# Kernel optimization log

Measured on AMD Instinct MI355X. Metric: run time of the kernel, lower is better.

## Reference

```python
import jax, jax.numpy as jnp
import numpy as np

N_NODES = 50000
N_EDGES = 800000
IN_F = 512
OUT_F = 96
ALPHA = 0.1
ITERATIONS = 10
AVG_DEG = 16


def setup_inputs() -> dict:
    key = jax.random.key(0)
    k1, k2, k3, k4, k5 = jax.random.split(key, 5)
    x = jax.random.normal(k1, (N_NODES, IN_F), dtype=jnp.float32)
    # xavier_uniform with gain=1.414 over [IN_F, OUT_F]
    limit = 1.414 * np.sqrt(6.0 / (IN_F + OUT_F))
    weight = jax.random.uniform(k2, (IN_F, OUT_F), dtype=jnp.float32,
                                minval=-limit, maxval=limit)
    edge_src = jax.random.randint(k3, (N_EDGES,), 0, N_NODES, dtype=jnp.int32)
    edge_dst = jax.random.randint(k4, (N_EDGES,), 0, N_NODES, dtype=jnp.int32)
    # values scaled like a row-normalized adjacency for stable propagation
    edge_val = jax.random.uniform(k5, (N_EDGES,), dtype=jnp.float32) / AVG_DEG
    return {"x": x, "weight": weight, "edge_src": edge_src,
            "edge_dst": edge_dst, "edge_val": edge_val}


def _spmm(edge_src, edge_dst, edge_val, h):
    # out[i] = sum_{edges e with dst=i} val[e] * h[src[e]]
    gathered = h[edge_src] * edge_val[:, None]          # [E, OUT_F]
    return jax.ops.segment_sum(gathered, edge_dst, num_segments=N_NODES)


def reference(x, weight, edge_src, edge_dst, edge_val):
    support = x @ weight                                 # [N, OUT_F]
    prev = support
    def body(_, s):
        s = _spmm(edge_src, edge_dst, edge_val, s) * (1.0 - ALPHA) + prev * ALPHA
        return jax.nn.relu(s)
    return jax.lax.fori_loop(0, ITERATIONS, body, support)
```

## Files before the change

kernel.cpp:

```cpp
#include <hip/hip_runtime.h>

typedef unsigned int   uint;
typedef unsigned short ushort;
typedef __attribute__((ext_vector_type(8))) short bf16x8;
typedef __attribute__((ext_vector_type(4))) float f32x4;

#define N_NODES 50000
#define N_EDGES 800000
#define IN_F    512
#define OUT_F   96
#define SCAN_BLOCKS 196
#define TPN 12
#define DEGBINS 256

__device__ __forceinline__ float bflo(uint u) { return __uint_as_float(u << 16); }
__device__ __forceinline__ float bfhi(uint u) { return __uint_as_float(u & 0xffff0000u); }
__device__ __forceinline__ uint f2bf(float x) {
    uint u = __float_as_uint(x);
    return (u + 0x7fffu + ((u >> 16) & 1u)) >> 16;
}
__device__ __forceinline__ uint pack2bf(float lo, float hi) {
    return f2bf(lo) | (f2bf(hi) << 16);
}

__global__ __launch_bounds__(256) void wt_kernel(const float* __restrict__ w,
                                                 ushort* __restrict__ wTp) {
    int t = blockIdx.x * 256 + threadIdx.x;
    if (t < IN_F * OUT_F) {
        int k = t / OUT_F, c = t - k * OUT_F;
        wTp[(size_t)(k >> 5) * (OUT_F * 32) + c * 32 + (k & 31)] =
            (ushort)f2bf(w[t]);
    }
}

__global__ __launch_bounds__(64) void gemm_kernel(const float* __restrict__ x,
                                                  const ushort* __restrict__ wTp,
                                                  ushort* __restrict__ supB) {
    const int lane = threadIdx.x;
    const int m    = lane & 15;
    const int quad = lane >> 4;

    const int row  = blockIdx.x * 16 + m;
    const int arow = (row < N_NODES) ? row : (N_NODES - 1);
    const float*  xp = x + (size_t)arow * IN_F + quad * 8;
    const ushort* wp = wTp + (size_t)m * 32 + quad * 8;

    f32x4 acc[6];
    #pragma unroll
    for (int ct = 0; ct < 6; ++ct) acc[ct] = (f32x4){0.f, 0.f, 0.f, 0.f};

    float4 xA0 = *(const float4*)(xp);
    float4 xB0 = *(const float4*)(xp + 4);
    float4 xA1 = *(const float4*)(xp + 32);
    float4 xB1 = *(const float4*)(xp + 36);
    bf16x8 b[6];
    #pragma unroll
    for (int ct = 0; ct < 6; ++ct)
        b[ct] = *(const bf16x8*)(wp + ct * (16 * 32));

    #pragma unroll
    for (int it = 0; it < 16; ++it) {
        float4 nxa, nxb;
        bf16x8 nb[6];
        if (it + 2 < 16) {
            nxa = *(const float4*)(xp + (it + 2) * 32);
            nxb = *(const float4*)(xp + (it + 2) * 32 + 4);
        }
        if (it + 1 < 16) {
            const ushort* wpn = wp + (size_t)(it + 1) * (OUT_F * 32);
            #pragma unroll
            for (int ct = 0; ct < 6; ++ct)
                nb[ct] = *(const bf16x8*)(wpn + ct * (16 * 32));
        }
        union { uint u[4]; bf16x8 v; } af;
        af.u[0] = pack2bf(xA0.x, xA0.y); af.u[1] = pack2bf(xA0.z, xA0.w);
        af.u[2] = pack2bf(xB0.x, xB0.y); af.u[3] = pack2bf(xB0.z, xB0.w);
        #pragma unroll
        for (int ct = 0; ct < 6; ++ct)
            acc[ct] = __builtin_amdgcn_mfma_f32_16x16x32_bf16(af.v, b[ct],
                                                              acc[ct], 0, 0, 0);
        xA0 = xA1; xB0 = xB1; xA1 = nxa; xB1 = nxb;
        #pragma unroll
        for (int ct = 0; ct < 6; ++ct) b[ct] = nb[ct];
    }

    const int orow0 = blockIdx.x * 16 + quad * 4;
    #pragma unroll
    for (int ct = 0; ct < 6; ++ct) {
        #pragma unroll
        for (int r = 0; r < 4; ++r) {
            int gr = orow0 + r;
            if (gr < N_NODES)
                supB[(size_t)gr * OUT_F + ct * 16 + m] = (ushort)f2bf(acc[ct][r]);
        }
    }
}

__global__ void zero_kernel(int* __restrict__ p, int n) {
    int t = blockIdx.x * blockDim.x + threadIdx.x;
    if (t < n) p[t] = 0;
}

__global__ void hist_kernel(const int* __restrict__ dst, int* __restrict__ counts) {
    int e = blockIdx.x * blockDim.x + threadIdx.x;
    if (e < N_EDGES) atomicAdd(&counts[dst[e]], 1);
}

__global__ __launch_bounds__(256) void block_reduce_kernel(const int* __restrict__ counts,
                                                           int* __restrict__ blockSums) {
    __shared__ int s[256];
    int idx = blockIdx.x * 256 + threadIdx.x;
    s[threadIdx.x] = (idx < N_NODES) ? counts[idx] : 0;
    __syncthreads();
    for (int off = 128; off > 0; off >>= 1) {
        if (threadIdx.x < off) s[threadIdx.x] += s[threadIdx.x + off];
        __syncthreads();
    }
    if (threadIdx.x == 0) blockSums[blockIdx.x] = s[0];
}

__global__ __launch_bounds__(256) void scan_sums_kernel(int* __restrict__ blockSums,
                                                        int* __restrict__ blockOffs,
                                                        int* __restrict__ rowstart) {
    __shared__ int s[256];
    int t = threadIdx.x;
    s[t] = (t < SCAN_BLOCKS) ? blockSums[t] : 0;
    __syncthreads();
    for (int off = 1; off < 256; off <<= 1) {
        int v = (t >= off) ? s[t - off] : 0;
        __syncthreads();
        s[t] += v;
        __syncthreads();
    }
    if (t < SCAN_BLOCKS) blockOffs[t] = (t == 0) ? 0 : s[t - 1];
    if (t == 0) rowstart[N_NODES] = s[SCAN_BLOCKS - 1];
}

__global__ __launch_bounds__(256) void block_scan_kernel(const int* __restrict__ counts,
                                                         const int* __restrict__ blockOffs,
                                                         int* __restrict__ rowstart,
                                                         int* __restrict__ cursor,
                                                         int* __restrict__ deghist) {
    __shared__ int s[256];
    __shared__ int lh[DEGBINS];
    int t   = threadIdx.x;
    int idx = blockIdx.x * 256 + t;
    int v   = (idx < N_NODES) ? counts[idx] : 0;
    s[t]  = v;
    lh[t] = 0;
    __syncthreads();
    for (int off = 1; off < 256; off <<= 1) {
        int u = (t >= off) ? s[t - off] : 0;
        __syncthreads();
        s[t] += u;
        __syncthreads();
    }
    if (idx < N_NODES) {
        int excl = blockOffs[blockIdx.x] + s[t] - v;
        rowstart[idx] = excl;
        cursor[idx]   = excl;
        int d = v < (DEGBINS - 1) ? v : (DEGBINS - 1);
        atomicAdd(&lh[d], 1);
    }
    __syncthreads();
    if (lh[t] > 0) atomicAdd(&deghist[t], lh[t]);
}

__global__ __launch_bounds__(256) void degscan_kernel(const int* __restrict__ deghist,
                                                      int* __restrict__ degcur) {
    __shared__ int s[256];
    int t = threadIdx.x;
    int v = deghist[t];
    s[t] = v;
    __syncthreads();
    for (int off = 1; off < 256; off <<= 1) {
        int u = (t >= off) ? s[t - off] : 0;
        __syncthreads();
        s[t] += u;
        __syncthreads();
    }
    degcur[t] = s[t] - v;
}

__global__ __launch_bounds__(256) void degscatter_kernel(const int* __restrict__ counts,
                                                         int* __restrict__ degcur,
                                                         int* __restrict__ perm) {
    __shared__ int lhist[DEGBINS];
    __shared__ int lbase[DEGBINS];
    int t = threadIdx.x;
    lhist[t] = 0;
    __syncthreads();
    int i = blockIdx.x * 256 + t;
    int d = 0, lr = 0;
    bool valid = (i < N_NODES);
    if (valid) {
        d  = counts[i];
        if (d > DEGBINS - 1) d = DEGBINS - 1;
        lr = atomicAdd(&lhist[d], 1);
    }
    __syncthreads();
    if (lhist[t] > 0) lbase[t] = atomicAdd(&degcur[t], lhist[t]);
    __syncthreads();
    if (valid) perm[lbase[d] + lr] = i;
}

__global__ void scatter_kernel(const int* __restrict__ src, const int* __restrict__ dst,
                               const float* __restrict__ val, int* __restrict__ cursor,
                               uint* __restrict__ edgeE) {
    int e = blockIdx.x * blockDim.x + threadIdx.x;
    if (e < N_EDGES) {
        int d   = dst[e];
        int pos = atomicAdd(&cursor[d], 1);
        edgeE[pos] = (f2bf(val[e]) << 16) | (uint)src[e];
    }
}

__device__ __forceinline__ void acc8(float* a, float v, uint4 hv) {
    a[0] = fmaf(v, bflo(hv.x), a[0]); a[1] = fmaf(v, bfhi(hv.x), a[1]);
    a[2] = fmaf(v, bflo(hv.y), a[2]); a[3] = fmaf(v, bfhi(hv.y), a[3]);
    a[4] = fmaf(v, bflo(hv.z), a[4]); a[5] = fmaf(v, bfhi(hv.z), a[5]);
    a[6] = fmaf(v, bflo(hv.w), a[6]); a[7] = fmaf(v, bfhi(hv.w), a[7]);
}

template <bool FINAL>
__global__ __launch_bounds__(256) void prop_kernel(const ushort* __restrict__ h,
                                                   const ushort* __restrict__ sup,
                                                   const int* __restrict__ rowstart,
                                                   const uint* __restrict__ edgeE,
                                                   const int* __restrict__ perm,
                                                   ushort* __restrict__ outB,
                                                   float* __restrict__ outF) {
    int t = blockIdx.x * 256 + threadIdx.x;
    int i = t / TPN;
    if (i >= N_NODES) return;
    int q = t - i * TPN;
    int f = q * 8;
    int node = perm[i];

    int start = rowstart[node];
    int end   = rowstart[node + 1];

    size_t o = (size_t)node * OUT_F + f;
    uint4 sp = *(const uint4*)(sup + o);

    float a[8] = {0.f, 0.f, 0.f, 0.f, 0.f, 0.f, 0.f, 0.f};
    int e  = start;
    int n8 = (end - start) >> 3;

    uint ed[8];
    if (n8 > 0) {
        #pragma unroll
        for (int u = 0; u < 8; ++u) ed[u] = edgeE[start + u];
    }
    for (int c = 0; c < n8; ++c) {
        uint4 hv[8];
        #pragma unroll
        for (int u = 0; u < 8; ++u)
            hv[u] = *(const uint4*)(h + (size_t)(ed[u] & 0xffffu) * OUT_F + f);
        uint edc[8];
        #pragma unroll
        for (int u = 0; u < 8; ++u) edc[u] = ed[u];
        if (c + 1 < n8) {
            #pragma unroll
            for (int u = 0; u < 8; ++u) ed[u] = edgeE[e + 8 + u];
        }
        #pragma unroll
        for (int u = 0; u < 8; ++u) acc8(a, bfhi(edc[u]), hv[u]);
        e += 8;
    }

    int rem = end - e;
    if (rem > 0) {
        uint edt[8];
        #pragma unroll
        for (int u = 0; u < 8; ++u) {
            int ee = e + u;
            edt[u] = edgeE[(ee < end) ? ee : (end - 1)];
        }
        uint4 hv[8];
        #pragma unroll
        for (int u = 0; u < 8; ++u)
            hv[u] = *(const uint4*)(h + (size_t)(edt[u] & 0xffffu) * OUT_F + f);
        #pragma unroll
        for (int u = 0; u < 8; ++u) {
            float v = (u < rem) ? bfhi(edt[u]) : 0.f;
            acc8(a, v, hv[u]);
        }
    }

    float r[8];
    r[0] = fmaxf(fmaf(a[0], 0.9f, bflo(sp.x) * 0.1f), 0.f);
    r[1] = fmaxf(fmaf(a[1], 0.9f, bfhi(sp.x) * 0.1f), 0.f);
    r[2] = fmaxf(fmaf(a[2], 0.9f, bflo(sp.y) * 0.1f), 0.f);
    r[3] = fmaxf(fmaf(a[3], 0.9f, bfhi(sp.y) * 0.1f), 0.f);
    r[4] = fmaxf(fmaf(a[4], 0.9f, bflo(sp.z) * 0.1f), 0.f);
    r[5] = fmaxf(fmaf(a[5], 0.9f, bfhi(sp.z) * 0.1f), 0.f);
    r[6] = fmaxf(fmaf(a[6], 0.9f, bflo(sp.w) * 0.1f), 0.f);
    r[7] = fmaxf(fmaf(a[7], 0.9f, bfhi(sp.w) * 0.1f), 0.f);

    if (FINAL) {
        *(float4*)(outF + o)     = make_float4(r[0], r[1], r[2], r[3]);
        *(float4*)(outF + o + 4) = make_float4(r[4], r[5], r[6], r[7]);
    } else {
        *(uint4*)(outB + o) = make_uint4(pack2bf(r[0], r[1]), pack2bf(r[2], r[3]),
                                         pack2bf(r[4], r[5]), pack2bf(r[6], r[7]));
    }
}

extern "C" void kernel_launch(void* const* d_in, const int* in_sizes, int n_in,
                              void* d_out, int out_size, void* d_ws, size_t ws_size,
                              hipStream_t stream) {
    const float* x    = (const float*)d_in[0];
    const float* w    = (const float*)d_in[1];
    const int*   esrc = (const int*)d_in[2];
    const int*   edst = (const int*)d_in[3];
    const float* eval = (const float*)d_in[4];
    float* out = (float*)d_out;

    const size_t supBytes = (size_t)N_NODES * OUT_F * sizeof(ushort);
    ushort* supB = (ushort*)d_out;
    ushort* wTp  = (ushort*)((char*)d_out + (size_t)out_size * 4
                             - (size_t)IN_F * OUT_F * sizeof(ushort));

    char*  xb  = (char*)d_in[0];
    size_t off = 0;
    auto alloc = [&](size_t bytes) -> char* {
        char* p = xb + off;
        off = (off + bytes + 255) & ~(size_t)255;
        return p;
    };
    ushort* supP      = (ushort*)alloc(supBytes);
    ushort* hU        = (ushort*)alloc(supBytes);
    ushort* hV        = (ushort*)alloc(supBytes);
    uint*   edgeE     = (uint*)alloc((size_t)N_EDGES * sizeof(uint));
    int*    rowstart  = (int*)alloc((N_NODES + 1) * sizeof(int));
    int*    cursor    = (int*)alloc(N_NODES * sizeof(int));
    int*    counts    = (int*)alloc((N_NODES + DEGBINS) * sizeof(int));
    int*    deghist   = counts + N_NODES;
    int*    blockSums = (int*)alloc(SCAN_BLOCKS * sizeof(int));
    int*    blockOffs = (int*)alloc(SCAN_BLOCKS * sizeof(int));
    int*    degcur    = (int*)alloc(DEGBINS * sizeof(int));
    int*    perm      = (int*)alloc(N_NODES * sizeof(int));

    wt_kernel<<<(IN_F * OUT_F + 255) / 256, 256, 0, stream>>>(w, wTp);

    gemm_kernel<<<(N_NODES + 15) / 16, 64, 0, stream>>>(x, wTp, supB);

    hipMemcpyAsync(supP, supB, supBytes, hipMemcpyDeviceToDevice, stream);

    zero_kernel<<<(N_NODES + DEGBINS + 255) / 256, 256, 0, stream>>>(
        counts, N_NODES + DEGBINS);
    hist_kernel<<<(N_EDGES + 255) / 256, 256, 0, stream>>>(edst, counts);
    block_reduce_kernel<<<SCAN_BLOCKS, 256, 0, stream>>>(counts, blockSums);
    scan_sums_kernel<<<1, 256, 0, stream>>>(blockSums, blockOffs, rowstart);
    block_scan_kernel<<<SCAN_BLOCKS, 256, 0, stream>>>(counts, blockOffs,
                                                       rowstart, cursor, deghist);
    degscan_kernel<<<1, 256, 0, stream>>>(deghist, degcur);
    degscatter_kernel<<<SCAN_BLOCKS, 256, 0, stream>>>(counts, degcur, perm);
    scatter_kernel<<<(N_EDGES + 255) / 256, 256, 0, stream>>>(esrc, edst, eval,
                                                              cursor, edgeE);

    const int pgrid = (N_NODES * TPN + 255) / 256;
    const ushort* in = supP;
    for (int it = 1; it <= 9; ++it) {
        ushort* o = (it & 1) ? hU : hV;
        prop_kernel<false><<<pgrid, 256, 0, stream>>>(in, supP, rowstart, edgeE,
                                                      perm, o, nullptr);
        in = o;
    }
    prop_kernel<true><<<pgrid, 256, 0, stream>>>(in, supP, rowstart, edgeE,
                                                 perm, nullptr, out);
}
```

Baseline: 535.2 us.

## Split feature columns into two grid halves and use nontemporal loads/stores

The propagation grid is split into two halves. Each half handles 48 of the 96 feature columns for every node, using 6 threads per node instead of 12, so all blocks working on one feature half run in sequence and that half of the h working set (about 4.8MB) stays resident in cache. Edge metadata, support loads and output stores switch to nontemporal hints so they do not evict the gathered h rows. The cost is that edge lists and rowstart are read twice, once per half.

```diff
diff --git a/kernel.cpp b/kernel.cpp
--- a/kernel.cpp
+++ b/kernel.cpp
@@ -4,13 +4,15 @@
 typedef unsigned short ushort;
 typedef __attribute__((ext_vector_type(8))) short bf16x8;
 typedef __attribute__((ext_vector_type(4))) float f32x4;
+typedef __attribute__((ext_vector_type(4))) uint  u32x4;
 
 #define N_NODES 50000
 #define N_EDGES 800000
 #define IN_F    512
 #define OUT_F   96
 #define SCAN_BLOCKS 196
-#define TPN 12
+#define HTPN 6
+#define HB   1172
 #define DEGBINS 256
 
 __device__ __forceinline__ float bflo(uint u) { return __uint_as_float(u << 16); }
@@ -22,6 +24,11 @@
 __device__ __forceinline__ uint pack2bf(float lo, float hi) {
     return f2bf(lo) | (f2bf(hi) << 16);
 }
+
+__device__ __forceinline__ uint  ntld1(const uint* p)  { return __builtin_nontemporal_load(p); }
+__device__ __forceinline__ u32x4 ntld4(const u32x4* p) { return __builtin_nontemporal_load(p); }
+__device__ __forceinline__ void  ntst4(u32x4* p, u32x4 v)  { __builtin_nontemporal_store(v, p); }
+__device__ __forceinline__ void  ntstf4(f32x4* p, f32x4 v) { __builtin_nontemporal_store(v, p); }
 
 __global__ __launch_bounds__(256) void wt_kernel(const float* __restrict__ w,
                                                  ushort* __restrict__ wTp) {
@@ -215,7 +222,7 @@
     }
 }
 
-__device__ __forceinline__ void acc8(float* a, float v, uint4 hv) {
+__device__ __forceinline__ void acc8(float* a, float v, u32x4 hv) {
     a[0] = fmaf(v, bflo(hv.x), a[0]); a[1] = fmaf(v, bfhi(hv.x), a[1]);
     a[2] = fmaf(v, bflo(hv.y), a[2]); a[3] = fmaf(v, bfhi(hv.y), a[3]);
     a[4] = fmaf(v, bflo(hv.z), a[4]); a[5] = fmaf(v, bfhi(hv.z), a[5]);
@@ -230,18 +237,19 @@
                                                    const int* __restrict__ perm,
                                                    ushort* __restrict__ outB,
                                                    float* __restrict__ outF) {
-    int t = blockIdx.x * 256 + threadIdx.x;
-    int i = t / TPN;
+    int half = (blockIdx.x >= HB) ? 1 : 0;
+    int t = (blockIdx.x - half * HB) * 256 + threadIdx.x;
+    int i = t / HTPN;
     if (i >= N_NODES) return;
-    int q = t - i * TPN;
-    int f = q * 8;
+    int q = t - i * HTPN;
+    int f = half * 48 + q * 8;
     int node = perm[i];
 
     int start = rowstart[node];
     int end   = rowstart[node + 1];
 
     size_t o = (size_t)node * OUT_F + f;
-    uint4 sp = *(const uint4*)(sup + o);
+    u32x4 sp = ntld4((const u32x4*)(sup + o));
 
     float a[8] = {0.f, 0.f, 0.f, 0.f, 0.f, 0.f, 0.f, 0.f};
     int e  = start;
@@ -250,19 +258,19 @@
     uint ed[8];
     if (n8 > 0) {
         #pragma unroll
-        for (int u = 0; u < 8; ++u) ed[u] = edgeE[start + u];
+        for (int u = 0; u < 8; ++u) ed[u] = ntld1(&edgeE[start + u]);
     }
     for (int c = 0; c < n8; ++c) {
-        uint4 hv[8];
+        u32x4 hv[8];
         #pragma unroll
         for (int u = 0; u < 8; ++u)
-            hv[u] = *(const uint4*)(h + (size_t)(ed[u] & 0xffffu) * OUT_F + f);
+            hv[u] = *(const u32x4*)(h + (size_t)(ed[u] & 0xffffu) * OUT_F + f);
         uint edc[8];
         #pragma unroll
         for (int u = 0; u < 8; ++u) edc[u] = ed[u];
         if (c + 1 < n8) {
             #pragma unroll
-            for (int u = 0; u < 8; ++u) ed[u] = edgeE[e + 8 + u];
+            for (int u = 0; u < 8; ++u) ed[u] = ntld1(&edgeE[e + 8 + u]);
         }
         #pragma unroll
         for (int u = 0; u < 8; ++u) acc8(a, bfhi(edc[u]), hv[u]);
@@ -275,12 +283,12 @@
         #pragma unroll
         for (int u = 0; u < 8; ++u) {
             int ee = e + u;
-            edt[u] = edgeE[(ee < end) ? ee : (end - 1)];
-        }
-        uint4 hv[8];
+            edt[u] = ntld1(&edgeE[(ee < end) ? ee : (end - 1)]);
+        }
+        u32x4 hv[8];
         #pragma unroll
         for (int u = 0; u < 8; ++u)
-            hv[u] = *(const uint4*)(h + (size_t)(edt[u] & 0xffffu) * OUT_F + f);
+            hv[u] = *(const u32x4*)(h + (size_t)(edt[u] & 0xffffu) * OUT_F + f);
         #pragma unroll
         for (int u = 0; u < 8; ++u) {
             float v = (u < rem) ? bfhi(edt[u]) : 0.f;
@@ -299,11 +307,12 @@
     r[7] = fmaxf(fmaf(a[7], 0.9f, bfhi(sp.w) * 0.1f), 0.f);
 
     if (FINAL) {
-        *(float4*)(outF + o)     = make_float4(r[0], r[1], r[2], r[3]);
-        *(float4*)(outF + o + 4) = make_float4(r[4], r[5], r[6], r[7]);
+        ntstf4((f32x4*)(outF + o),     (f32x4){r[0], r[1], r[2], r[3]});
+        ntstf4((f32x4*)(outF + o + 4), (f32x4){r[4], r[5], r[6], r[7]});
     } else {
-        *(uint4*)(outB + o) = make_uint4(pack2bf(r[0], r[1]), pack2bf(r[2], r[3]),
-                                         pack2bf(r[4], r[5]), pack2bf(r[6], r[7]));
+        ntst4((u32x4*)(outB + o),
+              (u32x4){pack2bf(r[0], r[1]), pack2bf(r[2], r[3]),
+                      pack2bf(r[4], r[5]), pack2bf(r[6], r[7])});
     }
 }
 
@@ -346,7 +355,7 @@
 
     gemm_kernel<<<(N_NODES + 15) / 16, 64, 0, stream>>>(x, wTp, supB);
 
-    hipMemcpyAsync(supP, supB, supBytes, hipMemcpyDeviceToDevice, stream);
+    (void)hipMemcpyAsync(supP, supB, supBytes, hipMemcpyDeviceToDevice, stream);
 
     zero_kernel<<<(N_NODES + DEGBINS + 255) / 256, 256, 0, stream>>>(
         counts, N_NODES + DEGBINS);
@@ -360,7 +369,7 @@
     scatter_kernel<<<(N_EDGES + 255) / 256, 256, 0, stream>>>(esrc, edst, eval,
                                                               cursor, edgeE);
 
-    const int pgrid = (N_NODES * TPN + 255) / 256;
+    const int pgrid = 2 * HB;
     const ushort* in = supP;
     for (int it = 1; it <= 9; ++it) {
         ushort* o = (it & 1) ? hU : hV;
```

Result: slower. 715.8 us (+33.7%).

## Split feature dimension into 32-wide panels and propagate each panel separately

Applied to the files above, without the earlier changes.

The support and hidden buffers are stored as three column panels of 32 features each, and every propagation iteration launches three kernels, one per panel, with 4 threads per node instead of 12. Each panel's gathered working set is 3.2MB instead of 9.6MB, so gathers should hit cache more often. In exchange, edge lists and rowstart are read three times per iteration and the number of kernel launches triples.

```diff
diff --git a/kernel.cpp b/kernel.cpp
--- a/kernel.cpp
+++ b/kernel.cpp
@@ -10,7 +10,9 @@
 #define IN_F    512
 #define OUT_F   96
 #define SCAN_BLOCKS 196
-#define TPN 12
+#define PTPN 4
+#define PB   782
+#define PANEL_ELEMS ((size_t)N_NODES * 32)
 #define DEGBINS 256
 
 __device__ __forceinline__ float bflo(uint u) { return __uint_as_float(u << 16); }
@@ -87,11 +89,15 @@
     const int orow0 = blockIdx.x * 16 + quad * 4;
     #pragma unroll
     for (int ct = 0; ct < 6; ++ct) {
+        const int col = ct * 16 + m;
+        const int p   = col >> 5;
+        const int pc  = col & 31;
         #pragma unroll
         for (int r = 0; r < 4; ++r) {
             int gr = orow0 + r;
             if (gr < N_NODES)
-                supB[(size_t)gr * OUT_F + ct * 16 + m] = (ushort)f2bf(acc[ct][r]);
+                supB[(size_t)p * PANEL_ELEMS + (size_t)gr * 32 + pc] =
+                    (ushort)f2bf(acc[ct][r]);
         }
     }
 }
@@ -229,18 +235,19 @@
                                                    const uint* __restrict__ edgeE,
                                                    const int* __restrict__ perm,
                                                    ushort* __restrict__ outB,
-                                                   float* __restrict__ outF) {
+                                                   float* __restrict__ outF,
+                                                   int panel) {
     int t = blockIdx.x * 256 + threadIdx.x;
-    int i = t / TPN;
+    int i = t >> 2;
     if (i >= N_NODES) return;
-    int q = t - i * TPN;
+    int q = t & 3;
     int f = q * 8;
     int node = perm[i];
 
     int start = rowstart[node];
     int end   = rowstart[node + 1];
 
-    size_t o = (size_t)node * OUT_F + f;
+    size_t o = (size_t)node * 32 + f;
     uint4 sp = *(const uint4*)(sup + o);
 
     float a[8] = {0.f, 0.f, 0.f, 0.f, 0.f, 0.f, 0.f, 0.f};
@@ -256,7 +263,7 @@
         uint4 hv[8];
         #pragma unroll
         for (int u = 0; u < 8; ++u)
-            hv[u] = *(const uint4*)(h + (size_t)(ed[u] & 0xffffu) * OUT_F + f);
+            hv[u] = *(const uint4*)(h + (size_t)(ed[u] & 0xffffu) * 32 + f);
         uint edc[8];
         #pragma unroll
         for (int u = 0; u < 8; ++u) edc[u] = ed[u];
@@ -280,7 +287,7 @@
         uint4 hv[8];
         #pragma unroll
         for (int u = 0; u < 8; ++u)
-            hv[u] = *(const uint4*)(h + (size_t)(edt[u] & 0xffffu) * OUT_F + f);
+            hv[u] = *(const uint4*)(h + (size_t)(edt[u] & 0xffffu) * 32 + f);
         #pragma unroll
         for (int u = 0; u < 8; ++u) {
             float v = (u < rem) ? bfhi(edt[u]) : 0.f;
@@ -299,8 +306,9 @@
     r[7] = fmaxf(fmaf(a[7], 0.9f, bfhi(sp.w) * 0.1f), 0.f);
 
     if (FINAL) {
-        *(float4*)(outF + o)     = make_float4(r[0], r[1], r[2], r[3]);
-        *(float4*)(outF + o + 4) = make_float4(r[4], r[5], r[6], r[7]);
+        float* op = outF + (size_t)node * OUT_F + panel * 32 + f;
+        *(float4*)(op)     = make_float4(r[0], r[1], r[2], r[3]);
+        *(float4*)(op + 4) = make_float4(r[4], r[5], r[6], r[7]);
     } else {
         *(uint4*)(outB + o) = make_uint4(pack2bf(r[0], r[1]), pack2bf(r[2], r[3]),
                                          pack2bf(r[4], r[5]), pack2bf(r[6], r[7]));
@@ -346,7 +354,7 @@
 
     gemm_kernel<<<(N_NODES + 15) / 16, 64, 0, stream>>>(x, wTp, supB);
 
-    hipMemcpyAsync(supP, supB, supBytes, hipMemcpyDeviceToDevice, stream);
+    (void)hipMemcpyAsync(supP, supB, supBytes, hipMemcpyDeviceToDevice, stream);
 
     zero_kernel<<<(N_NODES + DEGBINS + 255) / 256, 256, 0, stream>>>(
         counts, N_NODES + DEGBINS);
@@ -360,14 +368,19 @@
     scatter_kernel<<<(N_EDGES + 255) / 256, 256, 0, stream>>>(esrc, edst, eval,
                                                               cursor, edgeE);
 
-    const int pgrid = (N_NODES * TPN + 255) / 256;
     const ushort* in = supP;
     for (int it = 1; it <= 9; ++it) {
         ushort* o = (it & 1) ? hU : hV;
-        prop_kernel<false><<<pgrid, 256, 0, stream>>>(in, supP, rowstart, edgeE,
-                                                      perm, o, nullptr);
+        for (int p = 0; p < 3; ++p) {
+            prop_kernel<false><<<PB, 256, 0, stream>>>(
+                in + p * PANEL_ELEMS, supP + p * PANEL_ELEMS, rowstart, edgeE,
+                perm, o + p * PANEL_ELEMS, nullptr, p);
+        }
         in = o;
     }
-    prop_kernel<true><<<pgrid, 256, 0, stream>>>(in, supP, rowstart, edgeE,
-                                                 perm, nullptr, out);
-}
+    for (int p = 0; p < 3; ++p) {
+        prop_kernel<true><<<PB, 256, 0, stream>>>(
+            in + p * PANEL_ELEMS, supP + p * PANEL_ELEMS, rowstart, edgeE,
+            perm, nullptr, out, p);
+    }
+}
```

Result: slower. 639.7 us (+19.5%).
